# Kernel optimization log

Measured on AMD Instinct MI355X. Metric: run time of the kernel, lower is better.

Reference implementation:

```python
import jax, jax.numpy as jnp
import numpy as np

EPS = float(np.finfo(np.float32).eps)
H = 256          # hidden_size
K = 10           # num_event_types
B, S = 32, 4096  # batch, seq_len


def _linear_params(kw, kb, fan_in, fan_out):
    # torch nn.Linear default init (uniform +-1/sqrt(fan_in)), then abs + clamp(min=eps)
    bound = 1.0 / np.sqrt(fan_in)
    w = jnp.clip(jnp.abs(jax.random.uniform(kw, (fan_out, fan_in), minval=-bound, maxval=bound, dtype=jnp.float32)), EPS)
    b = jnp.clip(jnp.abs(jax.random.uniform(kb, (fan_out,), minval=-bound, maxval=bound, dtype=jnp.float32)), EPS)
    return w, b


def setup_inputs() -> dict:
    key = jax.random.key(0)
    ks = jax.random.split(key, 12)
    w1, b1 = _linear_params(ks[0], ks[1], 1, H)        # layer_dense_1
    w2, b2 = _linear_params(ks[2], ks[3], 2 * H, H)    # layer_dense_2
    wA, bA = _linear_params(ks[4], ks[5], H, H)        # module_list[0]
    wB, bB = _linear_params(ks[6], ks[7], H, H)        # module_list[1]
    w3, b3 = _linear_params(ks[8], ks[9], H, K)        # layer_dense_3 linear
    hidden_states = jax.random.normal(ks[10], (B, S, H), dtype=jnp.float32)
    time_delta_seqs = jax.random.uniform(ks[11], (B, S), dtype=jnp.float32)
    return dict(hidden_states=hidden_states, time_delta_seqs=time_delta_seqs,
                w1=w1, b1=b1, w2=w2, b2=b2, wA=wA, bA=bA, wB=wB, bB=bB, w3=w3, b3=b3)


def _cumul_hazard(td, h, w1, b1, w2, b2, wA, bA, wB, bB, w3, b3):
    # layer_dense_1: Linear(1 -> H) on td[..., None]
    t = td[..., None] * w1[:, 0] + b1                      # [B,S,H]
    out = jnp.tanh(jnp.concatenate([h, t], axis=-1) @ w2.T + b2)  # [B,S,H]
    out = jnp.tanh(out @ wA.T + bA)
    out = jnp.tanh(out @ wB.T + bB)
    return jax.nn.softplus(out @ w3.T + b3)                # [B,S,K]


def reference(hidden_states, time_delta_seqs, w1, b1, w2, b2, wA, bA, wB, bB, w3, b3):
    f = lambda td: _cumul_hazard(td, hidden_states, w1, b1, w2, b2, wA, bA, wB, bB, w3, b3)
    # Each output element depends only on its own t[b,s] (elementwise in time),
    # so a single forward-mode JVP with tangent=ones yields the exact per-element
    # derivative for ALL event types at once (fuses torch's per-type grad loop).
    integral_lambda, d_dt = jax.jvp(f, (time_delta_seqs,), (jnp.ones_like(time_delta_seqs),))
    # torch takes grad of .mean() over [B,S], which scales the derivative by 1/(B*S)
    derivative_integral_lambda = d_dt / time_delta_seqs.size
    return integral_lambda, derivative_integral_lambda
```

## Files before the change

### kernel.cpp

```cpp
#include <hip/hip_runtime.h>
#include <hip/hip_bf16.h>
#include <stdint.h>

typedef __bf16 bf16x8 __attribute__((ext_vector_type(8)));
typedef __bf16 bf16x4 __attribute__((ext_vector_type(4)));
typedef float  f32x4  __attribute__((ext_vector_type(4)));
typedef float  f32x2  __attribute__((ext_vector_type(2)));

#define MFMA16(a,b,c) __builtin_amdgcn_mfma_f32_16x16x32_bf16((a),(b),(c),0,0,0)

static constexpr int H_   = 256;
static constexpr int KEV  = 10;
static constexpr int NTOK = 32 * 4096;

__device__ __forceinline__ float ptanh(float x){
    float t = x * x;
    float n = fmaf(t, t + 105.0f, 945.0f);
    float d = fmaf(t, fmaf(t, 15.0f, 420.0f), 945.0f);
    float r = x * n * __builtin_amdgcn_rcpf(d);
    return fminf(1.0f, fmaxf(-1.0f, r));
}

__device__ __forceinline__ bf16x8 cvtFrag(const float* p){
    f32x4 a = *(const f32x4*)p;
    f32x4 b = *(const f32x4*)(p + 4);
    bf16x8 r;
    #pragma unroll
    for (int j = 0; j < 4; ++j){ r[j] = (__bf16)a[j]; r[4 + j] = (__bf16)b[j]; }
    return r;
}

__global__ void prep_vc(const float* __restrict__ w1, const float* __restrict__ b1,
                        const float* __restrict__ w2, const float* __restrict__ b2,
                        float* __restrict__ vc){
    int j = blockIdx.x * 4 + (threadIdx.x >> 6);
    int l = threadIdx.x & 63;
    const float* row = w2 + (size_t)j * (2 * H_) + H_;
    float v = 0.f, cc = 0.f;
    #pragma unroll
    for (int i = 0; i < 4; ++i){
        int k = l + 64 * i;
        float w = row[k];
        v  += w * w1[k];
        cc += w * b1[k];
    }
    #pragma unroll
    for (int off = 32; off; off >>= 1){
        v  += __shfl_down(v,  off, 64);
        cc += __shfl_down(cc, off, 64);
    }
    if (l == 0){ vc[j] = v; vc[H_ + j] = cc + b2[j]; }
}

__global__ void prep_pack(const float* __restrict__ w2, const float* __restrict__ wA,
                          const float* __restrict__ wB, __hip_bfloat16* __restrict__ pk){
    int b  = blockIdx.x;
    int L  = b >> 4, n0 = b & 15;
    const float* W = (L == 0) ? w2 : ((L == 1) ? wA : wB);
    int K = (L == 0) ? 2 * H_ : H_;
    __hip_bfloat16* dst = pk + (size_t)b * 4096;
    int t = threadIdx.x;
    #pragma unroll
    for (int u = 0; u < 2; ++u){
        int slot = t * 2 + u;
        int s = slot >> 6, q = (slot >> 4) & 3, c = slot & 15;
        const float* src = W + (size_t)(n0 * 16 + c) * K + 32 * s + 8 * q;
        #pragma unroll
        for (int j = 0; j < 8; ++j) dst[slot * 8 + j] = __float2bfloat16(src[j]);
    }
}

__global__ __launch_bounds__(256, 2) void chfn_kernel(
    const float* __restrict__ hs, const float* __restrict__ td,
    const __hip_bfloat16* __restrict__ wpk,
    const float* __restrict__ bA, const float* __restrict__ bB,
    const float* __restrict__ w3, const float* __restrict__ b3,
    const float* __restrict__ vc,
    float* __restrict__ out)
{
    __shared__ __hip_bfloat16 sA[4 * 16 * H_];
    __shared__ __hip_bfloat16 sD[4 * 16 * H_];

    const int tid  = threadIdx.x;
    const int wave = tid >> 6;
    const int lane = tid & 63;
    const int q    = lane >> 4;
    const int c    = lane & 15;
    const int tb   = blockIdx.x * 64 + wave * 16;
    const int wrow = wave * 16;

    const bf16x8* wp = (const bf16x8*)wpk;
    const int ws = q * 16 + c;

    bf16x8 W0[8], W1[8];
    {
        const bf16x8* b = wp + ws;
        #pragma unroll
        for (int s = 0; s < 8; ++s) W0[s] = b[s * 64];
    }

    bf16x8 aF[8], aB[8];
    {
        const float* h0 = hs + (size_t)(tb + c) * H_ + 8 * q;
        #pragma unroll
        for (int s = 0; s < 8; ++s) aF[s] = cvtFrag(h0 + 32 * s);
    }
    float myTd = td[tb + c];

    #pragma unroll 2
    for (int n0 = 0; n0 < 16; ++n0){
        bf16x8* cur = (n0 & 1) ? W1 : W0;
        bf16x8* nxt = (n0 & 1) ? W0 : W1;
        {
            const bf16x8* b = wp + (size_t)(n0 + 1) * 512 + ws;
            #pragma unroll
            for (int s = 0; s < 8; ++s) nxt[s] = b[s * 64];
        }
        f32x4 v4 = *(const f32x4*)(vc + n0 * 16 + 4 * q);
        f32x4 c4 = *(const f32x4*)(vc + H_ + n0 * 16 + 4 * q);
        f32x4 fa = c4;
        f32x4 fb = {0.f,0.f,0.f,0.f};
        #pragma unroll
        for (int s = 0; s < 4; ++s){
            fa = MFMA16(cur[s],     aF[s],     fa);
            fb = MFMA16(cur[s + 4], aF[s + 4], fb);
        }
        bf16x4 pa, pd;
        #pragma unroll
        for (int r = 0; r < 4; ++r){
            float x  = fmaf(myTd, v4[r], fa[r] + fb[r]);
            float th = ptanh(x);
            float dd = fmaf(-th, th, 1.0f) * v4[r];
            pa[r] = (__bf16)th; pd[r] = (__bf16)dd;
        }
        int off = (wrow + c) * H_ + (((2 * n0 + (q >> 1) + c) & 31) << 3) + ((q & 1) << 2);
        *(bf16x4*)((void*)(sA + off)) = pa;
        *(bf16x4*)((void*)(sD + off)) = pd;
    }

    #pragma unroll 1
    for (int L = 0; L < 2; ++L){
        const float* bias = L ? bB : bA;
        {
            const __hip_bfloat16* a0 = sA + (wrow + c) * H_;
            const __hip_bfloat16* d0 = sD + (wrow + c) * H_;
            #pragma unroll
            for (int s = 0; s < 8; ++s){
                int chn = (((4 * s + q) + c) & 31) << 3;
                aF[s] = *(const bf16x8*)(a0 + chn);
                aB[s] = *(const bf16x8*)(d0 + chn);
            }
        }
        #pragma unroll 2
        for (int n0 = 0; n0 < 16; ++n0){
            int g = 16 * (L + 1) + n0;
            bf16x8* cur = (n0 & 1) ? W1 : W0;
            bf16x8* nxt = (n0 & 1) ? W0 : W1;
            {
                int gn = g + 1; if (gn > 47) gn = 47;
                const bf16x8* b = wp + (size_t)gn * 512 + ws;
                #pragma unroll
                for (int s = 0; s < 8; ++s) nxt[s] = b[s * 64];
            }
            f32x4 b4 = *(const f32x4*)(bias + n0 * 16 + 4 * q);
            f32x4 fa = b4;
            f32x4 fb = {0.f,0.f,0.f,0.f};
            f32x4 ga = {0.f,0.f,0.f,0.f};
            f32x4 gb = {0.f,0.f,0.f,0.f};
            #pragma unroll
            for (int s = 0; s < 4; ++s){
                fa = MFMA16(cur[s],     aF[s],     fa);
                ga = MFMA16(cur[s],     aB[s],     ga);
                fb = MFMA16(cur[s + 4], aF[s + 4], fb);
                gb = MFMA16(cur[s + 4], aB[s + 4], gb);
            }
            bf16x4 pa, pd;
            #pragma unroll
            for (int r = 0; r < 4; ++r){
                float th = ptanh(fa[r] + fb[r]);
                float dd = fmaf(-th, th, 1.0f) * (ga[r] + gb[r]);
                pa[r] = (__bf16)th; pd[r] = (__bf16)dd;
            }
            int off = (wrow + c) * H_ + (((2 * n0 + (q >> 1) + c) & 31) << 3) + ((q & 1) << 2);
            *(bf16x4*)((void*)(sA + off)) = pa;
            *(bf16x4*)((void*)(sD + off)) = pd;
        }
    }

    {
        const __hip_bfloat16* a0 = sA + (wrow + c) * H_;
        const __hip_bfloat16* d0 = sD + (wrow + c) * H_;
        #pragma unroll
        for (int s = 0; s < 8; ++s){
            int chn = (((4 * s + q) + c) & 31) << 3;
            aF[s] = *(const bf16x8*)(a0 + chn);
            aB[s] = *(const bf16x8*)(d0 + chn);
        }
        int crow = (c < KEV) ? c : 0;
        const float* wp3 = w3 + (size_t)crow * H_ + 8 * q;
        f32x4 fa = {0.f,0.f,0.f,0.f}, fb = {0.f,0.f,0.f,0.f};
        f32x4 ga = {0.f,0.f,0.f,0.f}, gb = {0.f,0.f,0.f,0.f};
        #pragma unroll
        for (int s = 0; s < 4; ++s){
            bf16x8 bv0 = cvtFrag(wp3 + 32 * s);
            bf16x8 bv1 = cvtFrag(wp3 + 32 * (s + 4));
            fa = MFMA16(bv0, aF[s],     fa);
            ga = MFMA16(bv0, aB[s],     ga);
            fb = MFMA16(bv1, aF[s + 4], fb);
            gb = MFMA16(bv1, aB[s + 4], gb);
        }
        int fbase = 4 * q;
        size_t token = tb + c;
        float sp[4], dv[4];
        #pragma unroll
        for (int r = 0; r < 4; ++r){
            int fi   = fbase + r;
            float bn = b3[(fi < KEV) ? fi : (KEV - 1)];
            float z  = (fa[r] + fb[r]) + bn;
            float a  = fabsf(z);
            float e  = __builtin_amdgcn_exp2f(-1.4426950408889634f * a);
            sp[r] = fmaxf(z, 0.f) + 0.69314718055994531f * __builtin_amdgcn_logf(1.0f + e);
            float sg = __builtin_amdgcn_rcpf(1.0f + e);
            sg = (z >= 0.f) ? sg : 1.0f - sg;
            dv[r] = sg * (ga[r] + gb[r]) * (1.0f / 131072.0f);
        }
        float* o0 = out + token * KEV + fbase;
        float* o1 = out + (size_t)NTOK * KEV + token * KEV + fbase;
        if (q < 2){
            *(f32x2*)o0       = (f32x2){sp[0], sp[1]};
            *(f32x2*)(o0 + 2) = (f32x2){sp[2], sp[3]};
            *(f32x2*)o1       = (f32x2){dv[0], dv[1]};
            *(f32x2*)(o1 + 2) = (f32x2){dv[2], dv[3]};
        } else if (q == 2){
            *(f32x2*)o0 = (f32x2){sp[0], sp[1]};
            *(f32x2*)o1 = (f32x2){dv[0], dv[1]};
        }
    }
}

extern "C" void kernel_launch(void* const* d_in, const int* in_sizes, int n_in,
                              void* d_out, int out_size, void* d_ws, size_t ws_size,
                              hipStream_t stream){
    const float* hs = (const float*)d_in[0];
    const float* td = (const float*)d_in[1];
    const float* w1 = (const float*)d_in[2];
    const float* b1 = (const float*)d_in[3];
    const float* w2 = (const float*)d_in[4];
    const float* b2 = (const float*)d_in[5];
    const float* wA = (const float*)d_in[6];
    const float* bA = (const float*)d_in[7];
    const float* wB = (const float*)d_in[8];
    const float* bB = (const float*)d_in[9];
    const float* w3 = (const float*)d_in[10];
    const float* b3 = (const float*)d_in[11];

    float*          vc  = (float*)d_ws;
    __hip_bfloat16* wpk = (__hip_bfloat16*)((char*)d_ws + 4096);
    float*          outp = (float*)d_out;

    prep_vc  <<<64, 256, 0, stream>>>(w1, b1, w2, b2, vc);
    prep_pack<<<48, 256, 0, stream>>>(w2, wA, wB, wpk);
    chfn_kernel<<<NTOK / 64, 256, 0, stream>>>(hs, td, wpk, bA, bB, w3, b3, vc, outp);
}
```

Before: 330.6 us.

## Split output features across waves so each wave streams a quarter of weights

Instead of each wave handling 16 tokens and streaming all 256 output features of every layer's weights, the block now handles 32 tokens. Each wave computes a 64-feature slice for both 16-token groups, exchanging activations through shared memory with block-wide barriers between layers. This cuts per-wave weight fetch traffic by about 4x. In exchange it adds __syncthreads, doubles the grid size, and leaves two waves idle in the final projection.

Measured after the change: 392.6 us. 18.8% more time.

```diff
diff --git a/kernel.cpp b/kernel.cpp
--- a/kernel.cpp
+++ b/kernel.cpp
@@ -78,123 +78,142 @@
     const float* __restrict__ vc,
     float* __restrict__ out)
 {
-    __shared__ __hip_bfloat16 sA[4 * 16 * H_];
-    __shared__ __hip_bfloat16 sD[4 * 16 * H_];
+    __shared__ __hip_bfloat16 sA[32 * H_];
+    __shared__ __hip_bfloat16 sD[32 * H_];
 
     const int tid  = threadIdx.x;
     const int wave = tid >> 6;
     const int lane = tid & 63;
     const int q    = lane >> 4;
     const int c    = lane & 15;
-    const int tb   = blockIdx.x * 64 + wave * 16;
-    const int wrow = wave * 16;
+    const int tb   = blockIdx.x * 32;
 
     const bf16x8* wp = (const bf16x8*)wpk;
     const int ws = q * 16 + c;
 
-    bf16x8 W0[8], W1[8];
+    bf16x8 Wbuf[2][8];
     {
-        const bf16x8* b = wp + ws;
-        #pragma unroll
-        for (int s = 0; s < 8; ++s) W0[s] = b[s * 64];
-    }
-
-    bf16x8 aF[8], aB[8];
-    {
-        const float* h0 = hs + (size_t)(tb + c) * H_ + 8 * q;
-        #pragma unroll
-        for (int s = 0; s < 8; ++s) aF[s] = cvtFrag(h0 + 32 * s);
-    }
-    float myTd = td[tb + c];
-
-    #pragma unroll 2
-    for (int n0 = 0; n0 < 16; ++n0){
-        bf16x8* cur = (n0 & 1) ? W1 : W0;
-        bf16x8* nxt = (n0 & 1) ? W0 : W1;
+        const bf16x8* b = wp + (size_t)(4 * wave) * 512 + ws;
+        #pragma unroll
+        for (int s = 0; s < 8; ++s) Wbuf[0][s] = b[s * 64];
+    }
+
+    bf16x8 aF[2][8], aB[2][8];
+    #pragma unroll
+    for (int tg = 0; tg < 2; ++tg){
+        const float* h0 = hs + (size_t)(tb + 16 * tg + c) * H_ + 8 * q;
+        #pragma unroll
+        for (int s = 0; s < 8; ++s) aF[tg][s] = cvtFrag(h0 + 32 * s);
+    }
+    float tdg[2] = { td[tb + c], td[tb + 16 + c] };
+
+    #pragma unroll
+    for (int n0 = 0; n0 < 4; ++n0){
+        bf16x8* cur = Wbuf[n0 & 1];
+        bf16x8* nxt = Wbuf[(n0 + 1) & 1];
         {
-            const bf16x8* b = wp + (size_t)(n0 + 1) * 512 + ws;
+            int gn = (n0 < 3) ? (4 * wave + n0 + 1) : (16 + 4 * wave);
+            const bf16x8* b = wp + (size_t)gn * 512 + ws;
             #pragma unroll
             for (int s = 0; s < 8; ++s) nxt[s] = b[s * 64];
         }
-        f32x4 v4 = *(const f32x4*)(vc + n0 * 16 + 4 * q);
-        f32x4 c4 = *(const f32x4*)(vc + H_ + n0 * 16 + 4 * q);
-        f32x4 fa = c4;
-        f32x4 fb = {0.f,0.f,0.f,0.f};
-        #pragma unroll
-        for (int s = 0; s < 4; ++s){
-            fa = MFMA16(cur[s],     aF[s],     fa);
-            fb = MFMA16(cur[s + 4], aF[s + 4], fb);
-        }
-        bf16x4 pa, pd;
-        #pragma unroll
-        for (int r = 0; r < 4; ++r){
-            float x  = fmaf(myTd, v4[r], fa[r] + fb[r]);
-            float th = ptanh(x);
-            float dd = fmaf(-th, th, 1.0f) * v4[r];
-            pa[r] = (__bf16)th; pd[r] = (__bf16)dd;
-        }
-        int off = (wrow + c) * H_ + (((2 * n0 + (q >> 1) + c) & 31) << 3) + ((q & 1) << 2);
-        *(bf16x4*)((void*)(sA + off)) = pa;
-        *(bf16x4*)((void*)(sD + off)) = pd;
-    }
+        int fb0 = 64 * wave + 16 * n0;
+        f32x4 v4 = *(const f32x4*)(vc + fb0 + 4 * q);
+        f32x4 c4 = *(const f32x4*)(vc + H_ + fb0 + 4 * q);
+        int chn = 8 * wave + 2 * n0 + (q >> 1);
+        #pragma unroll
+        for (int tg = 0; tg < 2; ++tg){
+            f32x4 fa = c4;
+            f32x4 fb = {0.f,0.f,0.f,0.f};
+            #pragma unroll
+            for (int s = 0; s < 4; ++s){
+                fa = MFMA16(cur[s],     aF[tg][s],     fa);
+                fb = MFMA16(cur[s + 4], aF[tg][s + 4], fb);
+            }
+            bf16x4 pa, pd;
+            #pragma unroll
+            for (int r = 0; r < 4; ++r){
+                float x  = fmaf(tdg[tg], v4[r], fa[r] + fb[r]);
+                float th = ptanh(x);
+                float dd = fmaf(-th, th, 1.0f) * v4[r];
+                pa[r] = (__bf16)th; pd[r] = (__bf16)dd;
+            }
+            int row = 16 * tg + c;
+            int off = row * H_ + (((chn + row) & 31) << 3) + ((q & 1) << 2);
+            *(bf16x4*)((void*)(sA + off)) = pa;
+            *(bf16x4*)((void*)(sD + off)) = pd;
+        }
+    }
+    __syncthreads();
 
     #pragma unroll 1
-    for (int L = 0; L < 2; ++L){
-        const float* bias = L ? bB : bA;
-        {
-            const __hip_bfloat16* a0 = sA + (wrow + c) * H_;
-            const __hip_bfloat16* d0 = sD + (wrow + c) * H_;
+    for (int L = 1; L <= 2; ++L){
+        const float* bias = (L == 1) ? bA : bB;
+        #pragma unroll
+        for (int tg = 0; tg < 2; ++tg){
+            int row = 16 * tg + c;
+            const __hip_bfloat16* a0 = sA + row * H_;
+            const __hip_bfloat16* d0 = sD + row * H_;
             #pragma unroll
             for (int s = 0; s < 8; ++s){
-                int chn = (((4 * s + q) + c) & 31) << 3;
-                aF[s] = *(const bf16x8*)(a0 + chn);
-                aB[s] = *(const bf16x8*)(d0 + chn);
-            }
-        }
-        #pragma unroll 2
-        for (int n0 = 0; n0 < 16; ++n0){
-            int g = 16 * (L + 1) + n0;
-            bf16x8* cur = (n0 & 1) ? W1 : W0;
-            bf16x8* nxt = (n0 & 1) ? W0 : W1;
+                int chn = (((4 * s + q) + row) & 31) << 3;
+                aF[tg][s] = *(const bf16x8*)(a0 + chn);
+                aB[tg][s] = *(const bf16x8*)(d0 + chn);
+            }
+        }
+        __syncthreads();
+        #pragma unroll
+        for (int n0 = 0; n0 < 4; ++n0){
+            bf16x8* cur = Wbuf[n0 & 1];
+            bf16x8* nxt = Wbuf[(n0 + 1) & 1];
             {
-                int gn = g + 1; if (gn > 47) gn = 47;
+                int gn = (n0 < 3) ? (16 * L + 4 * wave + n0 + 1) : (16 * (L + 1) + 4 * wave);
+                if (gn > 47) gn = 47;
                 const bf16x8* b = wp + (size_t)gn * 512 + ws;
                 #pragma unroll
                 for (int s = 0; s < 8; ++s) nxt[s] = b[s * 64];
             }
-            f32x4 b4 = *(const f32x4*)(bias + n0 * 16 + 4 * q);
-            f32x4 fa = b4;
-            f32x4 fb = {0.f,0.f,0.f,0.f};
-            f32x4 ga = {0.f,0.f,0.f,0.f};
-            f32x4 gb = {0.f,0.f,0.f,0.f};
-            #pragma unroll
-            for (int s = 0; s < 4; ++s){
-                fa = MFMA16(cur[s],     aF[s],     fa);
-                ga = MFMA16(cur[s],     aB[s],     ga);
-                fb = MFMA16(cur[s + 4], aF[s + 4], fb);
-                gb = MFMA16(cur[s + 4], aB[s + 4], gb);
-            }
-            bf16x4 pa, pd;
-            #pragma unroll
-            for (int r = 0; r < 4; ++r){
-                float th = ptanh(fa[r] + fb[r]);
-                float dd = fmaf(-th, th, 1.0f) * (ga[r] + gb[r]);
-                pa[r] = (__bf16)th; pd[r] = (__bf16)dd;
-            }
-            int off = (wrow + c) * H_ + (((2 * n0 + (q >> 1) + c) & 31) << 3) + ((q & 1) << 2);
-            *(bf16x4*)((void*)(sA + off)) = pa;
-            *(bf16x4*)((void*)(sD + off)) = pd;
-        }
-    }
-
-    {
-        const __hip_bfloat16* a0 = sA + (wrow + c) * H_;
-        const __hip_bfloat16* d0 = sD + (wrow + c) * H_;
+            int fb0 = 64 * wave + 16 * n0;
+            f32x4 b4 = *(const f32x4*)(bias + fb0 + 4 * q);
+            int chn = 8 * wave + 2 * n0 + (q >> 1);
+            #pragma unroll
+            for (int tg = 0; tg < 2; ++tg){
+                f32x4 fa = b4;
+                f32x4 fb = {0.f,0.f,0.f,0.f};
+                f32x4 ga = {0.f,0.f,0.f,0.f};
+                f32x4 gb = {0.f,0.f,0.f,0.f};
+                #pragma unroll
+                for (int s = 0; s < 4; ++s){
+                    fa = MFMA16(cur[s],     aF[tg][s],     fa);
+                    ga = MFMA16(cur[s],     aB[tg][s],     ga);
+                    fb = MFMA16(cur[s + 4], aF[tg][s + 4], fb);
+                    gb = MFMA16(cur[s + 4], aB[tg][s + 4], gb);
+                }
+                bf16x4 pa, pd;
+                #pragma unroll
+                for (int r = 0; r < 4; ++r){
+                    float th = ptanh(fa[r] + fb[r]);
+                    float dd = fmaf(-th, th, 1.0f) * (ga[r] + gb[r]);
+                    pa[r] = (__bf16)th; pd[r] = (__bf16)dd;
+                }
+                int row = 16 * tg + c;
+                int off = row * H_ + (((chn + row) & 31) << 3) + ((q & 1) << 2);
+                *(bf16x4*)((void*)(sA + off)) = pa;
+                *(bf16x4*)((void*)(sD + off)) = pd;
+            }
+        }
+        __syncthreads();
+    }
+
+    if (wave < 2){
+        int row = 16 * wave + c;
+        const __hip_bfloat16* a0 = sA + row * H_;
+        const __hip_bfloat16* d0 = sD + row * H_;
         #pragma unroll
         for (int s = 0; s < 8; ++s){
-            int chn = (((4 * s + q) + c) & 31) << 3;
-            aF[s] = *(const bf16x8*)(a0 + chn);
-            aB[s] = *(const bf16x8*)(d0 + chn);
+            int chn = (((4 * s + q) + row) & 31) << 3;
+            aF[0][s] = *(const bf16x8*)(a0 + chn);
+            aB[0][s] = *(const bf16x8*)(d0 + chn);
         }
         int crow = (c < KEV) ? c : 0;
         const float* wp3 = w3 + (size_t)crow * H_ + 8 * q;
@@ -204,13 +223,13 @@
         for (int s = 0; s < 4; ++s){
             bf16x8 bv0 = cvtFrag(wp3 + 32 * s);
             bf16x8 bv1 = cvtFrag(wp3 + 32 * (s + 4));
-            fa = MFMA16(bv0, aF[s],     fa);
-            ga = MFMA16(bv0, aB[s],     ga);
-            fb = MFMA16(bv1, aF[s + 4], fb);
-            gb = MFMA16(bv1, aB[s + 4], gb);
+            fa = MFMA16(bv0, aF[0][s],     fa);
+            ga = MFMA16(bv0, aB[0][s],     ga);
+            fb = MFMA16(bv1, aF[0][s + 4], fb);
+            gb = MFMA16(bv1, aB[0][s + 4], gb);
         }
         int fbase = 4 * q;
-        size_t token = tb + c;
+        size_t token = tb + 16 * wave + c;
         float sp[4], dv[4];
         #pragma unroll
         for (int r = 0; r < 4; ++r){
@@ -260,5 +279,5 @@
 
     prep_vc  <<<64, 256, 0, stream>>>(w1, b1, w2, b2, vc);
     prep_pack<<<48, 256, 0, stream>>>(w2, wA, wB, wpk);
-    chfn_kernel<<<NTOK / 64, 256, 0, stream>>>(hs, td, wpk, bA, bB, w3, b3, vc, outp);
-}
+    chfn_kernel<<<NTOK / 32, 256, 0, stream>>>(hs, td, wpk, bA, bB, w3, b3, vc, outp);
+}
```

## Prepack w3 into bf16 tiles, shrink blocks to two waves, fix LDS swizzle

Applied to the files above, without the earlier changes.

Adds a 49th packed weight tile holding w3 in bf16 (zero-padded to 16 rows) and folds b3 into the vc buffer. The final layer can then reuse the double-buffered weight prefetch path instead of converting fp32 w3 rows inline in every wave. Blocks shrink from 4 waves to 2 (128 threads, launch bounds 3), halving shared memory per block to allow more resident blocks. The LDS swizzle changes from +c to +4c to reduce bank conflicts, and the tanh clamp uses fmed3. Smaller blocks may cost more launch and scheduling overhead, and three blocks per CU tightens the register budget.

Result: no change. 330.3 us (-0.1%).

```diff
diff --git a/kernel.cpp b/kernel.cpp
--- a/kernel.cpp
+++ b/kernel.cpp
@@ -18,7 +18,7 @@
     float n = fmaf(t, t + 105.0f, 945.0f);
     float d = fmaf(t, fmaf(t, 15.0f, 420.0f), 945.0f);
     float r = x * n * __builtin_amdgcn_rcpf(d);
-    return fminf(1.0f, fmaxf(-1.0f, r));
+    return __builtin_amdgcn_fmed3f(r, -1.0f, 1.0f);
 }
 
 __device__ __forceinline__ bf16x8 cvtFrag(const float* p){
@@ -32,7 +32,7 @@
 
 __global__ void prep_vc(const float* __restrict__ w1, const float* __restrict__ b1,
                         const float* __restrict__ w2, const float* __restrict__ b2,
-                        float* __restrict__ vc){
+                        const float* __restrict__ b3, float* __restrict__ vc){
     int j = blockIdx.x * 4 + (threadIdx.x >> 6);
     int l = threadIdx.x & 63;
     const float* row = w2 + (size_t)j * (2 * H_) + H_;
@@ -50,43 +50,52 @@
         cc += __shfl_down(cc, off, 64);
     }
     if (l == 0){ vc[j] = v; vc[H_ + j] = cc + b2[j]; }
+    if (blockIdx.x == 0 && threadIdx.x < 16)
+        vc[2 * H_ + threadIdx.x] = (threadIdx.x < KEV) ? b3[threadIdx.x] : 0.0f;
 }
 
 __global__ void prep_pack(const float* __restrict__ w2, const float* __restrict__ wA,
-                          const float* __restrict__ wB, __hip_bfloat16* __restrict__ pk){
+                          const float* __restrict__ wB, const float* __restrict__ w3,
+                          __hip_bfloat16* __restrict__ pk){
     int b  = blockIdx.x;
     int L  = b >> 4, n0 = b & 15;
-    const float* W = (L == 0) ? w2 : ((L == 1) ? wA : wB);
-    int K = (L == 0) ? 2 * H_ : H_;
+    const float* W; int K, nrows;
+    if (b == 48){ W = w3; K = H_; nrows = KEV; }
+    else { W = (L == 0) ? w2 : ((L == 1) ? wA : wB); K = (L == 0) ? 2 * H_ : H_; nrows = 16; }
     __hip_bfloat16* dst = pk + (size_t)b * 4096;
     int t = threadIdx.x;
     #pragma unroll
     for (int u = 0; u < 2; ++u){
         int slot = t * 2 + u;
         int s = slot >> 6, q = (slot >> 4) & 3, c = slot & 15;
-        const float* src = W + (size_t)(n0 * 16 + c) * K + 32 * s + 8 * q;
-        #pragma unroll
-        for (int j = 0; j < 8; ++j) dst[slot * 8 + j] = __float2bfloat16(src[j]);
-    }
-}
-
-__global__ __launch_bounds__(256, 2) void chfn_kernel(
+        int rr = (b == 48) ? c : (n0 * 16 + c);
+        if (c < nrows){
+            const float* src = W + (size_t)rr * K + 32 * s + 8 * q;
+            #pragma unroll
+            for (int j = 0; j < 8; ++j) dst[slot * 8 + j] = __float2bfloat16(src[j]);
+        } else {
+            #pragma unroll
+            for (int j = 0; j < 8; ++j) dst[slot * 8 + j] = __float2bfloat16(0.0f);
+        }
+    }
+}
+
+__global__ __launch_bounds__(128, 3) void chfn_kernel(
     const float* __restrict__ hs, const float* __restrict__ td,
     const __hip_bfloat16* __restrict__ wpk,
     const float* __restrict__ bA, const float* __restrict__ bB,
-    const float* __restrict__ w3, const float* __restrict__ b3,
     const float* __restrict__ vc,
     float* __restrict__ out)
 {
-    __shared__ __hip_bfloat16 sA[4 * 16 * H_];
-    __shared__ __hip_bfloat16 sD[4 * 16 * H_];
+    __shared__ __hip_bfloat16 sA[2 * 16 * H_];
+    __shared__ __hip_bfloat16 sD[2 * 16 * H_];
 
     const int tid  = threadIdx.x;
     const int wave = tid >> 6;
     const int lane = tid & 63;
     const int q    = lane >> 4;
     const int c    = lane & 15;
-    const int tb   = blockIdx.x * 64 + wave * 16;
+    const int tb   = blockIdx.x * 32 + wave * 16;
     const int wrow = wave * 16;
 
     const bf16x8* wp = (const bf16x8*)wpk;
@@ -133,7 +142,8 @@
             float dd = fmaf(-th, th, 1.0f) * v4[r];
             pa[r] = (__bf16)th; pd[r] = (__bf16)dd;
         }
-        int off = (wrow + c) * H_ + (((2 * n0 + (q >> 1) + c) & 31) << 3) + ((q & 1) << 2);
+        int chn = 2 * n0 + (q >> 1);
+        int off = (wrow + c) * H_ + (((chn + 4 * c) & 31) << 3) + ((q & 1) << 2);
         *(bf16x4*)((void*)(sA + off)) = pa;
         *(bf16x4*)((void*)(sD + off)) = pd;
     }
@@ -146,7 +156,7 @@
             const __hip_bfloat16* d0 = sD + (wrow + c) * H_;
             #pragma unroll
             for (int s = 0; s < 8; ++s){
-                int chn = (((4 * s + q) + c) & 31) << 3;
+                int chn = (((4 * s + q) + 4 * c) & 31) << 3;
                 aF[s] = *(const bf16x8*)(a0 + chn);
                 aB[s] = *(const bf16x8*)(d0 + chn);
             }
@@ -157,8 +167,7 @@
             bf16x8* cur = (n0 & 1) ? W1 : W0;
             bf16x8* nxt = (n0 & 1) ? W0 : W1;
             {
-                int gn = g + 1; if (gn > 47) gn = 47;
-                const bf16x8* b = wp + (size_t)gn * 512 + ws;
+                const bf16x8* b = wp + (size_t)(g + 1) * 512 + ws;
                 #pragma unroll
                 for (int s = 0; s < 8; ++s) nxt[s] = b[s * 64];
             }
@@ -181,7 +190,8 @@
                 float dd = fmaf(-th, th, 1.0f) * (ga[r] + gb[r]);
                 pa[r] = (__bf16)th; pd[r] = (__bf16)dd;
             }
-            int off = (wrow + c) * H_ + (((2 * n0 + (q >> 1) + c) & 31) << 3) + ((q & 1) << 2);
+            int chn = 2 * n0 + (q >> 1);
+            int off = (wrow + c) * H_ + (((chn + 4 * c) & 31) << 3) + ((q & 1) << 2);
             *(bf16x4*)((void*)(sA + off)) = pa;
             *(bf16x4*)((void*)(sD + off)) = pd;
         }
@@ -192,31 +202,29 @@
         const __hip_bfloat16* d0 = sD + (wrow + c) * H_;
         #pragma unroll
         for (int s = 0; s < 8; ++s){
-            int chn = (((4 * s + q) + c) & 31) << 3;
+            int chn = (((4 * s + q) + 4 * c) & 31) << 3;
             aF[s] = *(const bf16x8*)(a0 + chn);
             aB[s] = *(const bf16x8*)(d0 + chn);
         }
-        int crow = (c < KEV) ? c : 0;
-        const float* wp3 = w3 + (size_t)crow * H_ + 8 * q;
-        f32x4 fa = {0.f,0.f,0.f,0.f}, fb = {0.f,0.f,0.f,0.f};
-        f32x4 ga = {0.f,0.f,0.f,0.f}, gb = {0.f,0.f,0.f,0.f};
+        bf16x8* cur = W0;
+        f32x4 b4 = *(const f32x4*)(vc + 2 * H_ + 4 * q);
+        f32x4 fa = b4;
+        f32x4 fb = {0.f,0.f,0.f,0.f};
+        f32x4 ga = {0.f,0.f,0.f,0.f};
+        f32x4 gb = {0.f,0.f,0.f,0.f};
         #pragma unroll
         for (int s = 0; s < 4; ++s){
-            bf16x8 bv0 = cvtFrag(wp3 + 32 * s);
-            bf16x8 bv1 = cvtFrag(wp3 + 32 * (s + 4));
-            fa = MFMA16(bv0, aF[s],     fa);
-            ga = MFMA16(bv0, aB[s],     ga);
-            fb = MFMA16(bv1, aF[s + 4], fb);
-            gb = MFMA16(bv1, aB[s + 4], gb);
+            fa = MFMA16(cur[s],     aF[s],     fa);
+            ga = MFMA16(cur[s],     aB[s],     ga);
+            fb = MFMA16(cur[s + 4], aF[s + 4], fb);
+            gb = MFMA16(cur[s + 4], aB[s + 4], gb);
         }
         int fbase = 4 * q;
         size_t token = tb + c;
         float sp[4], dv[4];
         #pragma unroll
         for (int r = 0; r < 4; ++r){
-            int fi   = fbase + r;
-            float bn = b3[(fi < KEV) ? fi : (KEV - 1)];
-            float z  = (fa[r] + fb[r]) + bn;
+            float z  = fa[r] + fb[r];
             float a  = fabsf(z);
             float e  = __builtin_amdgcn_exp2f(-1.4426950408889634f * a);
             sp[r] = fmaxf(z, 0.f) + 0.69314718055994531f * __builtin_amdgcn_logf(1.0f + e);
@@ -258,7 +266,7 @@
     __hip_bfloat16* wpk = (__hip_bfloat16*)((char*)d_ws + 4096);
     float*          outp = (float*)d_out;
 
-    prep_vc  <<<64, 256, 0, stream>>>(w1, b1, w2, b2, vc);
-    prep_pack<<<48, 256, 0, stream>>>(w2, wA, wB, wpk);
-    chfn_kernel<<<NTOK / 64, 256, 0, stream>>>(hs, td, wpk, bA, bB, w3, b3, vc, outp);
-}
+    prep_vc  <<<64, 256, 0, stream>>>(w1, b1, w2, b2, b3, vc);
+    prep_pack<<<49, 256, 0, stream>>>(w2, wA, wB, w3, wpk);
+    chfn_kernel<<<NTOK / 32, 128, 0, stream>>>(hs, td, wpk, bA, bB, vc, outp);
+}
```
